# Kernel optimization log

Hardware: AMD Instinct MI355X
Metric: run time of the kernel (lower is better)

Reference implementation:

```python
import jax, jax.numpy as jnp
import numpy as np

N_NODES = 50000
E_G = 1600000   # edges of g = nodes of line graph h
E_H = 2000000   # edges of line graph h (triplets)
IN_FEATS = 64
N_COLORS = 4


def setup_inputs() -> dict:
    key = jax.random.key(0)
    k1, k2, k3, k4, k5, k6, k7, k8 = jax.random.split(key, 8)
    return {
        "h_nodes": jax.random.randint(k1, (N_NODES,), 0, N_COLORS, dtype=jnp.int32),
        "src_g": jax.random.randint(k2, (E_G,), 0, N_NODES, dtype=jnp.int32),
        "dst_g": jax.random.randint(k3, (E_G,), 0, N_NODES, dtype=jnp.int32),
        "src_h": jax.random.randint(k4, (E_H,), 0, E_G, dtype=jnp.int32),
        "dst_h": jax.random.randint(k5, (E_H,), 0, E_G, dtype=jnp.int32),
        "e1_w": jax.random.normal(k6, (2, IN_FEATS), dtype=jnp.float32),
        "e2_w": jax.random.normal(k7, (2, IN_FEATS), dtype=jnp.float32),
        "e3_w": jax.random.normal(k8, (2, IN_FEATS), dtype=jnp.float32),
    }


def reference(h_nodes, src_g, dst_g, src_h, dst_h, e1_w, e2_w, e3_w):
    # g.apply_edges(send_h_src): per g-edge gather of node colors
    h_src = h_nodes[src_g]   # [E_G] color at source node of each g-edge
    h_dst = h_nodes[dst_g]   # [E_G] color at dest node of each g-edge
    # line graph h: its nodes are g's edges; apply_edges(comparison3)
    ha = h_src[src_h]        # [E_H] src-edge's source color (a)
    hc = h_dst[dst_h]        # [E_H] dst-edge's dest color (c)
    hb = h_dst[src_h]        # [E_H] src-edge's dest color (b = shared node)
    hac = (ha == hc).astype(jnp.int32)
    hab = (ha == hb).astype(jnp.int32)
    hbc = (hc == hb).astype(jnp.int32)
    # three size-2 embedding lookups + sum -> [E_H, IN_FEATS]
    return e1_w[hac] + e2_w[hab] + e3_w[hbc]
```

## Files before the change

kernel.cpp:

```cpp
#include <hip/hip_runtime.h>
#include <hip/hip_bf16.h>

__global__ void pack_edge_colors_kernel(const int* __restrict__ src_g,
                                        const int* __restrict__ dst_g,
                                        const int* __restrict__ h_nodes,
                                        unsigned char* __restrict__ pc,
                                        int eg) {
    int stride = gridDim.x * blockDim.x;
    for (int e = blockIdx.x * blockDim.x + threadIdx.x; e < eg; e += stride) {
        int hs = h_nodes[src_g[e]];
        int hd = h_nodes[dst_g[e]];
        pc[e] = (unsigned char)((hs << 2) | hd);
    }
}

__global__ void __launch_bounds__(256)
triplet_out_kernel(const int* __restrict__ src_h,
                   const int* __restrict__ dst_h,
                   const unsigned char* __restrict__ pc,
                   const float* __restrict__ e1,
                   const float* __restrict__ e2,
                   const float* __restrict__ e3,
                   float4* __restrict__ out4,
                   int eh) {
    __shared__ float table[8 * 64];

    for (int i = threadIdx.x; i < 8 * 64; i += blockDim.x) {
        int combo = i >> 6;
        int f     = i & 63;
        float v = e1[((combo >> 2) & 1) * 64 + f]
                + e2[((combo >> 1) & 1) * 64 + f]
                + e3[( combo       & 1) * 64 + f];
        table[combo * 64 + f] = v;
    }
    __syncthreads();

    const float4* table4 = (const float4*)table;

    const int rows_per_blk = blockDim.x >> 4;
    const int lane16 = threadIdx.x & 15;
    const int rgrp   = threadIdx.x >> 4;
    const long long ntiles = ((long long)eh + rows_per_blk - 1) / rows_per_blk;

    for (long long tile = blockIdx.x; tile < ntiles; tile += gridDim.x) {
        long long row = tile * rows_per_blk + rgrp;
        if (row < eh) {
            int s = src_h[row];
            int d = dst_h[row];
            unsigned int ps = pc[s];
            unsigned int pd = pc[d];
            int a = (int)(ps >> 2);
            int b = (int)(ps & 3u);
            int c = (int)(pd & 3u);
            int combo = ((a == c) << 2) | ((a == b) << 1) | (int)(b == c);
            out4[row * 16 + lane16] = table4[combo * 16 + lane16];
        }
    }
}

extern "C" void kernel_launch(void* const* d_in, const int* in_sizes, int n_in,
                              void* d_out, int out_size, void* d_ws, size_t ws_size,
                              hipStream_t stream) {
    const int* h_nodes = (const int*)d_in[0];
    const int* src_g   = (const int*)d_in[1];
    const int* dst_g   = (const int*)d_in[2];
    const int* src_h   = (const int*)d_in[3];
    const int* dst_h   = (const int*)d_in[4];
    const float* e1_w  = (const float*)d_in[5];
    const float* e2_w  = (const float*)d_in[6];
    const float* e3_w  = (const float*)d_in[7];

    const int eg = in_sizes[1];
    const int eh = in_sizes[3];

    unsigned char* pc = (unsigned char*)d_ws;

    pack_edge_colors_kernel<<<2048, 256, 0, stream>>>(src_g, dst_g, h_nodes, pc, eg);

    triplet_out_kernel<<<2048, 256, 0, stream>>>(src_h, dst_h, pc,
                                                 e1_w, e2_w, e3_w,
                                                 (float4*)d_out, eh);
}
```

Measured before the change: 588.0 us.

## Compute triplet combos once per row into shared memory and vectorize edge packing

The triplet kernel no longer has each of 16 lanes redundantly load src/dst indices and gather packed colors per row. Each thread now computes one row's combo into a shared buffer, and the block then writes 256 rows of output cooperatively from the precomputed table. The pack kernel reads the edge index arrays as int4 and writes four color bytes per thread. The cost is two block barriers per tile.

```diff
diff --git a/kernel.cpp b/kernel.cpp
--- a/kernel.cpp
+++ b/kernel.cpp
@@ -1,18 +1,34 @@
 #include <hip/hip_runtime.h>
 #include <hip/hip_bf16.h>
 
-__global__ void pack_edge_colors_kernel(const int* __restrict__ src_g,
-                                        const int* __restrict__ dst_g,
-                                        const int* __restrict__ h_nodes,
-                                        unsigned char* __restrict__ pc,
-                                        int eg) {
-    int stride = gridDim.x * blockDim.x;
-    for (int e = blockIdx.x * blockDim.x + threadIdx.x; e < eg; e += stride) {
-        int hs = h_nodes[src_g[e]];
-        int hd = h_nodes[dst_g[e]];
-        pc[e] = (unsigned char)((hs << 2) | hd);
+__global__ void __launch_bounds__(256)
+pack_edge_colors_kernel(const int4* __restrict__ src_g4,
+                        const int4* __restrict__ dst_g4,
+                        const int* __restrict__ src_g,
+                        const int* __restrict__ dst_g,
+                        const int* __restrict__ h_nodes,
+                        unsigned char* __restrict__ pc,
+                        int eg) {
+    const int n4 = eg >> 2;
+    const int stride = gridDim.x * blockDim.x;
+    for (int i = blockIdx.x * blockDim.x + threadIdx.x; i < n4; i += stride) {
+        int4 s = src_g4[i];
+        int4 d = dst_g4[i];
+        uchar4 p;
+        p.x = (unsigned char)((h_nodes[s.x] << 2) | h_nodes[d.x]);
+        p.y = (unsigned char)((h_nodes[s.y] << 2) | h_nodes[d.y]);
+        p.z = (unsigned char)((h_nodes[s.z] << 2) | h_nodes[d.z]);
+        p.w = (unsigned char)((h_nodes[s.w] << 2) | h_nodes[d.w]);
+        *(uchar4*)(pc + (i << 2)) = p;
+    }
+    int t = blockIdx.x * blockDim.x + threadIdx.x;
+    int e = (n4 << 2) + t;
+    if (e < eg) {
+        pc[e] = (unsigned char)((h_nodes[src_g[e]] << 2) | h_nodes[dst_g[e]]);
     }
 }
+
+#define ROWS_PER_TILE 256
 
 __global__ void __launch_bounds__(256)
 triplet_out_kernel(const int* __restrict__ src_h,
@@ -24,26 +40,24 @@
                    float4* __restrict__ out4,
                    int eh) {
     __shared__ float table[8 * 64];
+    __shared__ unsigned char combo_s[ROWS_PER_TILE];
 
-    for (int i = threadIdx.x; i < 8 * 64; i += blockDim.x) {
+    const int tid = threadIdx.x;
+
+    for (int i = tid; i < 8 * 64; i += blockDim.x) {
         int combo = i >> 6;
         int f     = i & 63;
-        float v = e1[((combo >> 2) & 1) * 64 + f]
-                + e2[((combo >> 1) & 1) * 64 + f]
-                + e3[( combo       & 1) * 64 + f];
-        table[combo * 64 + f] = v;
+        table[i] = e1[((combo >> 2) & 1) * 64 + f]
+                 + e2[((combo >> 1) & 1) * 64 + f]
+                 + e3[( combo       & 1) * 64 + f];
     }
     __syncthreads();
 
     const float4* table4 = (const float4*)table;
 
-    const int rows_per_blk = blockDim.x >> 4;
-    const int lane16 = threadIdx.x & 15;
-    const int rgrp   = threadIdx.x >> 4;
-    const long long ntiles = ((long long)eh + rows_per_blk - 1) / rows_per_blk;
-
-    for (long long tile = blockIdx.x; tile < ntiles; tile += gridDim.x) {
-        long long row = tile * rows_per_blk + rgrp;
+    for (long long base = (long long)blockIdx.x * ROWS_PER_TILE; base < eh;
+         base += (long long)gridDim.x * ROWS_PER_TILE) {
+        long long row = base + tid;
         if (row < eh) {
             int s = src_h[row];
             int d = dst_h[row];
@@ -52,9 +66,19 @@
             int a = (int)(ps >> 2);
             int b = (int)(ps & 3u);
             int c = (int)(pd & 3u);
-            int combo = ((a == c) << 2) | ((a == b) << 1) | (int)(b == c);
-            out4[row * 16 + lane16] = table4[combo * 16 + lane16];
+            combo_s[tid] =
+                (unsigned char)(((a == c) << 2) | ((a == b) << 1) | (int)(b == c));
         }
+        __syncthreads();
+
+        int nrows = eh - base < ROWS_PER_TILE ? (int)(eh - base) : ROWS_PER_TILE;
+        int total4 = nrows << 4;
+        for (int j = tid; j < total4; j += blockDim.x) {
+            int rl   = j >> 4;
+            int lane = j & 15;
+            out4[(base + rl) * 16 + lane] = table4[combo_s[rl] * 16 + lane];
+        }
+        __syncthreads();
     }
 }
 
@@ -75,7 +99,8 @@
 
     unsigned char* pc = (unsigned char*)d_ws;
 
-    pack_edge_colors_kernel<<<2048, 256, 0, stream>>>(src_g, dst_g, h_nodes, pc, eg);
+    pack_edge_colors_kernel<<<2048, 256, 0, stream>>>(
+        (const int4*)src_g, (const int4*)dst_g, src_g, dst_g, h_nodes, pc, eg);
 
     triplet_out_kernel<<<2048, 256, 0, stream>>>(src_h, dst_h, pc,
                                                  e1_w, e2_w, e3_w,
```

New measurement: 561.2 us. 1.05x faster.
